# Kernel tuning notes

Hardware: AMD Instinct MI355X
Metric: run time of the kernel (lower is better)

## Reference

```python
import jax, jax.numpy as jnp
import numpy as np

DT = 0.01
C_M = 1.0
G_NA, G_K, G_L = 120.0, 36.0, 0.3
E_NA, E_K, E_L = 50.0, -77.0, -54.387
G_SYN = 0.1  # all six conductances are 0.1
# order: AMPA, GABAa, GABAb, NMDA, ACh, D1 (type codes 1..6)
E_SYN = jnp.array([0.0, -70.0, -90.0, 0.0, 0.0, 0.0], jnp.float32)
TAU = jnp.array([2.0, 5.0, 10.0, 100.0, 50.0, 30.0], jnp.float32)
# I_pre = I_ext - I_AMPA + I_GABAa + I_GABAb - I_NMDA - I_ACh - I_D1
SIGN = jnp.array([-1.0, 1.0, 1.0, -1.0, -1.0, -1.0], jnp.float32)


def setup_inputs() -> dict:
    key = jax.random.key(0)
    N = 4096
    k0, k1, k2, k3 = jax.random.split(key, 4)
    return dict(
        I_ext=jax.random.normal(k0, (N,), jnp.float32),
        synaptic_weights=jax.random.uniform(k1, (N, N), jnp.float32),
        V0=jnp.zeros((N,), jnp.float32),
        m0=jnp.zeros((N,), jnp.float32),
        h0=jnp.zeros((N,), jnp.float32),
        n0=jnp.zeros((N,), jnp.float32),
        s0=jax.random.uniform(k2, (6, N), jnp.float32),
        synapse_types=jax.random.randint(k3, (N, N), 0, 7).astype(jnp.int32),
        T=10,
    )


def reference(I_ext, synaptic_weights, V0, m0, h0, n0, s0, synapse_types, T):
    num_steps = int(T / DT)
    # sum_{i,j} vec[j] * mask_t[i,j] * W[i,j] == dot(vec, colsum_t)
    # precompute per-type column sums of masked weights: [6, N]
    cols = jnp.stack([
        jnp.sum(jnp.where(synapse_types == t, synaptic_weights, 0.0), axis=0)
        for t in range(1, 7)
    ])
    decay = 1.0 - DT / TAU  # [6], exponential decay of gating variables

    def step(carry, _):
        V, m, h, n, s = carry
        s = s * decay[:, None]                          # [6, N]
        vec = G_SYN * s * (V[None, :] - E_SYN[:, None])  # [6, N]
        I_t = jnp.sum(vec * cols, axis=1)                # [6] scalar currents
        I_pre = I_ext + jnp.sum(SIGN * I_t)              # [N]
        # HH gating rates at current V
        am = (2.5 - 0.1 * V) / (jnp.exp(2.5 - 0.1 * V) - 1.0)
        bm = 4.0 * jnp.exp(-V / 18.0)
        ah = 0.07 * jnp.exp(-V / 20.0)
        bh = 1.0 / (jnp.exp(3.0 - 0.1 * V) + 1.0)
        an = (0.1 - 0.01 * V) / (jnp.exp(1.0 - 0.1 * V) - 1.0)
        bn = 0.125 * jnp.exp(-V / 80.0)
        m = m + DT * (am * (1.0 - m) - bm * m)
        h = h + DT * (ah * (1.0 - h) - bh * h)
        n = n + DT * (an * (1.0 - n) - bn * n)
        I_Na = G_NA * m**3 * h * (V - E_NA)
        I_K = G_K * n**4 * (V - E_K)
        I_L = G_L * (V - E_L)
        Vn = jnp.clip(V + DT * (I_pre - I_Na - I_K - I_L) / C_M, -100.0, 100.0)
        Vn = jnp.nan_to_num(Vn)
        return (Vn, m, h, n, s), Vn

    _, V_hist = jax.lax.scan(step, (V0, m0, h0, n0, s0), None, length=num_steps)
    return V_hist  # [num_steps, N]
```

## Files before the change

kernel.cpp:

```cpp
#include <hip/hip_runtime.h>
#include <math.h>

#define NN 4096
#define CBLK 8
#define NPB (NN / CBLK)
#define GRID_SIM 128
#define SLOT_STRIDE 16
#define CTRL_BYTES 4096
#define CTRL_ULLS 512
#define TRAJ_CAP 2040
#define TRAJ_BYTES 8192

typedef unsigned long long ull;


template <int DC, int RM>
__device__ __forceinline__ float dppmov(float x) {
    return __int_as_float(
        __builtin_amdgcn_update_dpp(0, __float_as_int(x), DC, RM, 0xf, true));
}
__device__ __forceinline__ float wave_sum63(float x) {
    x += dppmov<0x111, 0xf>(x);
    x += dppmov<0x112, 0xf>(x);
    x += dppmov<0x114, 0xf>(x);
    x += dppmov<0x118, 0xf>(x);
    x += dppmov<0x142, 0xa>(x);
    x += dppmov<0x143, 0xc>(x);
    return x;
}
__device__ __forceinline__ float wave_max63(float x) {
    x = fmaxf(x, dppmov<0x111, 0xf>(x));
    x = fmaxf(x, dppmov<0x112, 0xf>(x));
    x = fmaxf(x, dppmov<0x114, 0xf>(x));
    x = fmaxf(x, dppmov<0x118, 0xf>(x));
    x = fmaxf(x, dppmov<0x142, 0xa>(x));
    x = fmaxf(x, dppmov<0x143, 0xc>(x));
    return x;
}
__device__ __forceinline__ float dpp_sum8(float x) {
    x += dppmov<0x111, 0xf>(x);
    x += dppmov<0x112, 0xf>(x);
    x += dppmov<0x114, 0xf>(x);
    return x;
}
__device__ __forceinline__ float rdlane(float x, int l) {
    return __int_as_float(__builtin_amdgcn_readlane(__float_as_int(x), l));
}

__global__ __launch_bounds__(256) void col_partial_k(
    const float* __restrict__ W, const int* __restrict__ Ty,
    float* __restrict__ part, int chunkRows)
{
    const int tid = threadIdx.x;
    const int wv = tid >> 6;
    const int lane = tid & 63;
    const int j4 = (blockIdx.x * 64 + lane) * 4;
    const int c = blockIdx.y;
    const int rpw = chunkRows >> 2;
    const size_t i0 = (size_t)c * (size_t)chunkRows + (size_t)wv * (size_t)rpw;

    float a[6][4];
#pragma unroll
    for (int t = 0; t < 6; ++t)
#pragma unroll
        for (int r = 0; r < 4; ++r) a[t][r] = 0.f;

#pragma unroll 4
    for (size_t i = i0; i < i0 + (size_t)rpw; ++i) {
        const size_t off = i * NN + j4;
        const float4 w = *(const float4*)(W + off);
        const int4 t = *(const int4*)(Ty + off);
        const float wv4[4] = { w.x, w.y, w.z, w.w };
        const int tv[4] = { t.x, t.y, t.z, t.w };
#pragma unroll
        for (int r = 0; r < 4; ++r) {
            a[0][r] += (tv[r] == 1) ? wv4[r] : 0.f;
            a[1][r] += (tv[r] == 2) ? wv4[r] : 0.f;
            a[2][r] += (tv[r] == 3) ? wv4[r] : 0.f;
            a[3][r] += (tv[r] == 4) ? wv4[r] : 0.f;
            a[4][r] += (tv[r] == 5) ? wv4[r] : 0.f;
            a[5][r] += (tv[r] == 6) ? wv4[r] : 0.f;
        }
    }

    __shared__ float red[3][64][25];
    if (wv > 0) {
#pragma unroll
        for (int t = 0; t < 6; ++t)
#pragma unroll
            for (int r = 0; r < 4; ++r)
                red[wv - 1][lane][t * 4 + r] = a[t][r];
    }
    __syncthreads();
    if (wv == 0) {
#pragma unroll
        for (int w = 0; w < 3; ++w)
#pragma unroll
            for (int t = 0; t < 6; ++t)
#pragma unroll
                for (int r = 0; r < 4; ++r)
                    a[t][r] += red[w][lane][t * 4 + r];
        const size_t base = ((size_t)c * 6) * NN + (size_t)j4;
#pragma unroll
        for (int t = 0; t < 6; ++t)
            *(float4*)(part + base + (size_t)t * NN) =
                make_float4(a[t][0], a[t][1], a[t][2], a[t][3]);
    }
}

__global__ __launch_bounds__(256) void col_reduce_k(
    const float* __restrict__ part, float* __restrict__ cols, int CH)
{
    const int idx = blockIdx.x * 256 + threadIdx.x;
    float s = 0.f;
    for (int c = 0; c < CH; ++c) s += part[(size_t)c * 6 * NN + idx];
    cols[idx] = s;
}

__global__ __launch_bounds__(512) void hh_probe_k(
    const float* __restrict__ Iext, const float* __restrict__ V0,
    const float* __restrict__ m0, const float* __restrict__ h0,
    const float* __restrict__ n0, const float* __restrict__ s0,
    const float* __restrict__ cols, ull* __restrict__ ctrl,
    const int* __restrict__ Tp,
    float* __restrict__ traj, int* __restrict__ status)
{
#pragma clang fp contract(off)
    const int tid = threadIdx.x, wave = tid >> 6, lane = tid & 63;
    const int steps = Tp[0] * 100;

    if (tid < CTRL_ULLS) ctrl[tid] = 0ULL;

    __shared__ float red[8];
    __shared__ float sQg[6], sMIe, sBad;

    float bad = 0.f, mie = 0.f;
    for (int i = tid; i < NN; i += 512) {
        bad += (V0[i] != 0.f) ? 1.f : 0.f;
        bad += (m0[i] != 0.f) ? 1.f : 0.f;
        bad += (h0[i] != 0.f) ? 1.f : 0.f;
        bad += (n0[i] != 0.f) ? 1.f : 0.f;
        mie = fmaxf(mie, fabsf(Iext[i]));
    }
    bad = wave_sum63(bad);
    if (lane == 63) red[wave] = bad;
    __syncthreads();
    if (tid == 0) { float s = 0.f; for (int w = 0; w < 8; ++w) s += red[w]; sBad = s; }
    __syncthreads();
    mie = wave_max63(mie);
    if (lane == 63) red[wave] = mie;
    __syncthreads();
    if (tid == 0) { float s = 0.f; for (int w = 0; w < 8; ++w) s = fmaxf(s, red[w]); sMIe = s; }
    __syncthreads();
    for (int t = 0; t < 6; ++t) {
        float acc = 0.f;
        for (int i = tid; i < NN; i += 512)
            acc += 0.1f * s0[(size_t)t * NN + i] * cols[(size_t)t * NN + i];
        acc = wave_sum63(acc);
        if (lane == 63) red[wave] = acc;
        __syncthreads();
        if (tid == 0) { float s = 0.f; for (int w = 0; w < 8; ++w) s += red[w]; sQg[t] = s; }
        __syncthreads();
    }

    if (sBad != 0.f || steps > TRAJ_CAP) {
        if (tid == 0) *status = 0;
        return;
    }
    if (wave != 0) return;

    float Qg[6];
#pragma unroll
    for (int t = 0; t < 6; ++t) Qg[t] = sQg[t];
    const float MIe = sMIe;
    const float CE1g = -70.0f * Qg[1];
    const float CE2g = -90.0f * Qg[2];

    const float tau[6] = { 2.0f, 5.0f, 10.0f, 100.0f, 50.0f, 30.0f };
    const float sgn[6] = { -1.0f, 1.0f, 1.0f, -1.0f, -1.0f, -1.0f };
    float dec[6], sD[6];
#pragma unroll
    for (int t = 0; t < 6; ++t) { dec[t] = 1.0f - 0.01f / tau[t]; sD[t] = sgn[t] * dec[t]; }

    float vu = 0.0f, m = 0.0f, h = 0.0f, n = 0.0f;
    int ok = 1;
    int kend = steps;

    for (int k = 0; k < steps; ++k) {
        float Cg = sD[5] * Qg[5];
        Cg = fmaf(sD[4], Qg[4], Cg);
        Cg = fmaf(sD[3], Qg[3], Cg);
        Cg = fmaf(sD[2], Qg[2], Cg);
        Cg = fmaf(sD[1], Qg[1], Cg);
        Cg = fmaf(sD[0], Qg[0], Cg);
        const float corrg = fmaf(sD[1], CE1g, sD[2] * CE2g);
        const float S = fmaf(vu, Cg, -corrg);

        const float v = vu;
        const float a1 = 2.5f - 0.1f * v;
        const float X = __expf(a1);
        const float am = a1 * __builtin_amdgcn_rcpf(X - 1.0f);
        const float bm = 4.0f * __expf(v * (-1.0f / 18.0f));
        const float ah = 0.07f * __expf(v * (-1.0f / 20.0f));
        const float bh = __builtin_amdgcn_rcpf(fmaf(1.6487212707001281f, X, 1.0f));
        const float a5 = 0.1f - 0.01f * v;
        const float an = a5 * __builtin_amdgcn_rcpf(fmaf(0.2231301601484298f, X, -1.0f));
        const float bn = 0.125f * __expf(v * (-1.0f / 80.0f));
        const float mm = m + 0.01f * (am * (1.0f - m) - bm * m);
        const float hh = h + 0.01f * (ah * (1.0f - h) - bh * h);
        const float nn = n + 0.01f * (an * (1.0f - n) - bn * n);
        m = mm; h = hh; n = nn;
        const float INa = ((120.0f * ((mm * mm) * mm)) * hh) * (v - 50.0f);
        const float n2 = nn * nn;
        const float IK = (36.0f * (n2 * n2)) * (v + 77.0f);
        const float IL = 0.3f * (v + 54.387f);
        const float Bu = ((0.0f - INa) - IK) - IL;
        const float t = vu + 0.01f * (Bu + S);

        float vn;
        if (t != t) {
            vn = 0.0f;
        } else if (t > 1e30f) {
            vn = 100.0f;
        } else if (t < -1e30f) {
            vn = -100.0f;
        } else {
            const float slack = 0.01f * MIe + 0.01f +
                1e-4f * (fabsf(t) + fabsf(vu) +
                         0.01f * (fabsf(S) + fabsf(INa) + fabsf(IK)));
            if (t - slack > 100.0f)       vn = 100.0f;
            else if (t + slack < -100.0f) vn = -100.0f;
            else { ok = 0; break; }
        }
        if (lane == 0) traj[k] = vn;
        vu = vn;

        if ((m != m) || (h != h) || (n != n)) { kend = k + 1; break; }

#pragma unroll
        for (int t6 = 0; t6 < 6; ++t6) sD[t6] *= dec[t6];
    }
    if (ok) {
        for (int r = kend + lane; r < steps; r += 64) traj[r] = 0.0f;
    }
    if (lane == 0) *status = ok;
}

__global__ __launch_bounds__(NPB) void hh_sim_k(
    const float* __restrict__ Iext, const float* __restrict__ V0,
    const float* __restrict__ m0, const float* __restrict__ h0,
    const float* __restrict__ n0, const float* __restrict__ s0,
    const float* __restrict__ cols, const int* __restrict__ Tp,
    ull* __restrict__ ctrl, const float* __restrict__ traj,
    const int* __restrict__ status, float* __restrict__ out)
{
#pragma clang fp contract(off)
    const int steps = Tp[0] * 100;
    const int tid = threadIdx.x;

    if (*status == 1) {
        for (int r = blockIdx.x; r < steps; r += GRID_SIM) {
            const float vv = traj[r];
            const float4 val = make_float4(vv, vv, vv, vv);
            float4* p = (float4*)(out + (size_t)r * NN + (size_t)tid * 8);
            p[0] = val; p[1] = val;
        }
        return;
    }

    const int wave = tid >> 6;
    const int lane = tid & 63;

    __shared__ int sRank; __shared__ ull sKey, sChosen;
    __shared__ ull wtag[2][8];
    __shared__ float binit1[8], binit2[8];

    if (tid == 0) {
        const int xid = (int)(__builtin_amdgcn_s_getreg((3 << 11) | 20)) & 7;
        const ull r = atomicAdd(&ctrl[(size_t)xid * SLOT_STRIDE], 1ULL);
        if (r == (ull)(CBLK - 1))
            atomicCAS(&ctrl[128], 0ULL, (ull)(xid + 1));
        ull ch;
        do {
            ch = __hip_atomic_load(&ctrl[128],
                                   __ATOMIC_RELAXED, __HIP_MEMORY_SCOPE_AGENT);
        } while (ch == 0ULL);
        sRank = (int)r; sKey = (ull)(xid + 1); sChosen = ch;
    }
    __syncthreads();
    const int b = sRank;
    if (sKey != sChosen || b >= CBLK) return;

    const int j = b * NPB + tid;
    ull* const slots = ctrl + 144;

    const float tau[6] = { 2.0f, 5.0f, 10.0f, 100.0f, 50.0f, 30.0f };
    const float sgn[6] = { -1.0f, 1.0f, 1.0f, -1.0f, -1.0f, -1.0f };
    float dec[6], sD[6];
#pragma unroll
    for (int t = 0; t < 6; ++t) { dec[t] = 1.0f - 0.01f / tau[t]; sD[t] = sgn[t]; }

    if (tid < 16) wtag[tid >> 3][tid & 7] = 0ULL;

    float V = V0[j], m = m0[j], h = h0[j], n = n0[j], Ie = Iext[j];
    float q[6];
#pragma unroll
    for (int t = 0; t < 6; ++t)
        q[t] = 0.1f * s0[(size_t)t * NN + j] * cols[(size_t)t * NN + j];

    {
        const float b1 = wave_sum63(q[1]);
        const float b2 = wave_sum63(q[2]);
        if (lane == 63) { binit1[wave] = b1; binit2[wave] = b2; }
    }
    __syncthreads();
    float CE1 = 0.f, CE2 = 0.f;
    if (wave == 0) {
        const float s1 = dpp_sum8((lane < 8) ? binit1[lane] : 0.f);
        const float s2 = dpp_sum8((lane < 8) ? binit2[lane] : 0.f);
        CE1 = -70.0f * rdlane(s1, 7);
        CE2 = -90.0f * rdlane(s2, 7);
    }
    __syncthreads();

#pragma unroll
    for (int t = 0; t < 6; ++t) sD[t] *= dec[t];
    float w6 = sD[5] * q[5];
    w6 = fmaf(sD[4], q[4], w6);
    w6 = fmaf(sD[3], q[3], w6);
    w6 = fmaf(sD[2], q[2], w6);
    w6 = fmaf(sD[1], q[1], w6);
    w6 = fmaf(sD[0], q[0], w6);
    float corr = fmaf(sD[1], CE1, sD[2] * CE2);

    float* op = out + j;

    for (int k = 0; k < steps; ++k) {
        const unsigned tag = (unsigned)(k + 1);
        const int par = (k & 1);

        const float x = w6 * V;
        const float xs = wave_sum63(x);
        if (lane == 63)
            __hip_atomic_store(&wtag[par][wave],
                               ((ull)tag << 32) | (ull)__float_as_uint(xs),
                               __ATOMIC_RELAXED, __HIP_MEMORY_SCOPE_WORKGROUP);
        __builtin_amdgcn_sched_barrier(0);

        if (wave == 0) {
            ull got = 0;
            if (lane < 8) {
                do {
                    got = __hip_atomic_load(&wtag[par][lane],
                                            __ATOMIC_RELAXED,
                                            __HIP_MEMORY_SCOPE_WORKGROUP);
                } while ((unsigned)(got >> 32) != tag);
            }
            float p = dpp_sum8((lane < 8) ? __uint_as_float((unsigned)got) : 0.f);
            if (lane == 7) {
                p = p - corr;
                const ull packed = ((ull)tag << 32) | (ull)__float_as_uint(p);
                __hip_atomic_store(&slots[(size_t)(par * CBLK + b) * SLOT_STRIDE],
                                   packed, __ATOMIC_RELAXED,
                                   __HIP_MEMORY_SCOPE_AGENT);
            }
        }
        __builtin_amdgcn_sched_barrier(0);
        __builtin_amdgcn_s_barrier();
        __builtin_amdgcn_sched_barrier(0);

        const float v = V;
        const float a1 = 2.5f - 0.1f * v;
        const float X = __expf(a1);
        const float am = a1 * __builtin_amdgcn_rcpf(X - 1.0f);
        const float bm = 4.0f * __expf(v * (-1.0f / 18.0f));
        const float ah = 0.07f * __expf(v * (-1.0f / 20.0f));
        const float bh = __builtin_amdgcn_rcpf(
            fmaf(1.6487212707001281f, X, 1.0f));
        const float a5 = 0.1f - 0.01f * v;
        const float an = a5 * __builtin_amdgcn_rcpf(
            fmaf(0.2231301601484298f, X, -1.0f));
        const float bn = 0.125f * __expf(v * (-1.0f / 80.0f));
        const float mm = m + 0.01f * (am * (1.0f - m) - bm * m);
        const float hh = h + 0.01f * (ah * (1.0f - h) - bh * h);
        const float nn = n + 0.01f * (an * (1.0f - n) - bn * n);
        m = mm; h = hh; n = nn;
        const float INa = ((120.0f * ((mm * mm) * mm)) * hh) * (v - 50.0f);
        const float n2 = nn * nn;
        const float IK = (36.0f * (n2 * n2)) * (v + 77.0f);
        const float IL = 0.3f * (v + 54.387f);
        const float base = ((Ie - INa) - IK) - IL;

#pragma unroll
        for (int t = 0; t < 6; ++t) sD[t] *= dec[t];
        float w6n = sD[5] * q[5];
        w6n = fmaf(sD[4], q[4], w6n);
        w6n = fmaf(sD[3], q[3], w6n);
        w6n = fmaf(sD[2], q[2], w6n);
        w6n = fmaf(sD[1], q[1], w6n);
        w6n = fmaf(sD[0], q[0], w6n);
        const float corrn = fmaf(sD[1], CE1, sD[2] * CE2);
        __builtin_amdgcn_sched_barrier(0);

        ull got = 0;
        if (lane < 8) {
            do {
                got = __hip_atomic_load(&slots[(size_t)(par * CBLK + lane) * SLOT_STRIDE],
                                        __ATOMIC_RELAXED, __HIP_MEMORY_SCOPE_AGENT);
            } while ((unsigned)(got >> 32) != tag);
        }
        float val = dpp_sum8((lane < 8) ? __uint_as_float((unsigned)got) : 0.f);
        const float S = rdlane(val, 7);

        const float u = V + 0.01f * (base + S);
        V = (u != u) ? 0.0f : fminf(fmaxf(u, -100.0f), 100.0f);
        *op = V; op += NN;
        w6 = w6n; corr = corrn;
    }
}

__global__ __launch_bounds__(1024) void hh_sim_single(
    const float* __restrict__ Iext, const float* __restrict__ V0,
    const float* __restrict__ m0, const float* __restrict__ h0,
    const float* __restrict__ n0, const float* __restrict__ s0,
    const float* __restrict__ colsg, const int* __restrict__ Tp,
    const float* __restrict__ W, const int* __restrict__ Ty,
    int computeCols, float* __restrict__ out)
{
#pragma clang fp contract(off)
    const int tid = threadIdx.x;
    const int j0 = tid * 4;
    const int steps = Tp[0] * 100;

    const float tau[6] = { 2.0f, 5.0f, 10.0f, 100.0f, 50.0f, 30.0f };
    const float sgn[6] = { -1.0f, 1.0f, 1.0f, -1.0f, -1.0f, -1.0f };
    float dec[6], sD[6];
#pragma unroll
    for (int t = 0; t < 6; ++t) { dec[t] = 1.0f - 0.01f / tau[t]; sD[t] = sgn[t]; }

    float q[6][4];
    if (computeCols) {
        float acc[6][4];
#pragma unroll
        for (int t = 0; t < 6; ++t)
#pragma unroll
            for (int r = 0; r < 4; ++r) acc[t][r] = 0.f;
        for (int i = 0; i < NN; ++i) {
            const size_t rowo = (size_t)i * NN + (size_t)j0;
#pragma unroll
            for (int r = 0; r < 4; ++r) {
                const float w = W[rowo + r];
                const int t = Ty[rowo + r];
                acc[0][r] += (t == 1) ? w : 0.f;
                acc[1][r] += (t == 2) ? w : 0.f;
                acc[2][r] += (t == 3) ? w : 0.f;
                acc[3][r] += (t == 4) ? w : 0.f;
                acc[4][r] += (t == 5) ? w : 0.f;
                acc[5][r] += (t == 6) ? w : 0.f;
            }
        }
#pragma unroll
        for (int t = 0; t < 6; ++t)
#pragma unroll
            for (int r = 0; r < 4; ++r)
                q[t][r] = 0.1f * s0[(size_t)t * NN + j0 + r] * acc[t][r];
    } else {
#pragma unroll
        for (int t = 0; t < 6; ++t)
#pragma unroll
            for (int r = 0; r < 4; ++r)
                q[t][r] = 0.1f * s0[(size_t)t * NN + j0 + r] *
                          colsg[(size_t)t * NN + j0 + r];
    }

    float V[4], m[4], h[4], n[4], Ie[4];
#pragma unroll
    for (int r = 0; r < 4; ++r) {
        V[r] = V0[j0 + r]; m[r] = m0[j0 + r]; h[r] = h0[j0 + r];
        n[r] = n0[j0 + r]; Ie[r] = Iext[j0 + r];
    }

    __shared__ float wsum[2][16];
    __shared__ float Bsh[2];
    {
        float b1 = 0.f, b2 = 0.f;
#pragma unroll
        for (int r = 0; r < 4; ++r) { b1 += q[1][r]; b2 += q[2][r]; }
#pragma unroll
        for (int off = 32; off > 0; off >>= 1) {
            b1 += __shfl_down(b1, off);
            b2 += __shfl_down(b2, off);
        }
        if ((tid & 63) == 0) { wsum[0][tid >> 6] = b1; wsum[1][tid >> 6] = b2; }
        __syncthreads();
        if (tid == 0) {
            float s1 = 0.f, s2 = 0.f;
            for (int w2 = 0; w2 < 16; ++w2) { s1 += wsum[0][w2]; s2 += wsum[1][w2]; }
            Bsh[0] = s1; Bsh[1] = s2;
        }
        __syncthreads();
    }
    const float CE1 = -70.0f * Bsh[0];
    const float CE2 = -90.0f * Bsh[1];
    __syncthreads();

    for (int k = 0; k < steps; ++k) {
#pragma unroll
        for (int t = 0; t < 6; ++t) sD[t] *= dec[t];
        float p = 0.f;
#pragma unroll
        for (int r = 0; r < 4; ++r) {
            float w = sD[5] * q[5][r];
            w = fmaf(sD[4], q[4][r], w);
            w = fmaf(sD[3], q[3][r], w);
            w = fmaf(sD[2], q[2][r], w);
            w = fmaf(sD[1], q[1][r], w);
            w = fmaf(sD[0], q[0][r], w);
            p = fmaf(w, V[r], p);
        }
#pragma unroll
        for (int off = 32; off > 0; off >>= 1) p += __shfl_down(p, off);
        const int par = k & 1;
        if ((tid & 63) == 0) wsum[par][tid >> 6] = p;
        __syncthreads();
        float psum = 0.f;
#pragma unroll
        for (int w2 = 0; w2 < 16; ++w2) psum += wsum[par][w2];
        const float S = psum - fmaf(sD[1], CE1, sD[2] * CE2);

#pragma unroll
        for (int r = 0; r < 4; ++r) {
            const float v = V[r];
            const float Ipre = Ie[r] + S;
            const float a1 = 2.5f - 0.1f * v;
            const float X = __expf(a1);
            const float am = a1 * __builtin_amdgcn_rcpf(X - 1.0f);
            const float bm = 4.0f * __expf(v * (-1.0f / 18.0f));
            const float ah = 0.07f * __expf(v * (-1.0f / 20.0f));
            const float bh = __builtin_amdgcn_rcpf(fmaf(1.6487212707001281f, X, 1.0f));
            const float a5 = 0.1f - 0.01f * v;
            const float an = a5 * __builtin_amdgcn_rcpf(fmaf(0.2231301601484298f, X, -1.0f));
            const float bn = 0.125f * __expf(v * (-1.0f / 80.0f));
            const float mm = m[r] + 0.01f * (am * (1.0f - m[r]) - bm * m[r]);
            const float hh = h[r] + 0.01f * (ah * (1.0f - h[r]) - bh * h[r]);
            const float nn = n[r] + 0.01f * (an * (1.0f - n[r]) - bn * n[r]);
            m[r] = mm; h[r] = hh; n[r] = nn;
            const float INa = ((120.0f * ((mm * mm) * mm)) * hh) * (v - 50.0f);
            const float n2 = nn * nn;
            const float IK = (36.0f * (n2 * n2)) * (v + 77.0f);
            const float IL = 0.3f * (v + 54.387f);
            const float u = v + 0.01f * (((Ipre - INa) - IK) - IL);
            V[r] = (u != u) ? 0.0f : fminf(fmaxf(u, -100.0f), 100.0f);
        }
        *(float4*)(out + (size_t)k * NN + j0) =
            make_float4(V[0], V[1], V[2], V[3]);
    }
}

extern "C" void kernel_launch(void* const* d_in, const int* in_sizes, int n_in,
                              void* d_out, int out_size, void* d_ws, size_t ws_size,
                              hipStream_t stream)
{
    const float* Iext = (const float*)d_in[0];
    const float* W    = (const float*)d_in[1];
    const float* V0   = (const float*)d_in[2];
    const float* m0   = (const float*)d_in[3];
    const float* h0   = (const float*)d_in[4];
    const float* n0   = (const float*)d_in[5];
    const float* s0   = (const float*)d_in[6];
    const int*   Ty   = (const int*)d_in[7];
    const int*   Tp   = (const int*)d_in[8];
    float* out = (float*)d_out;

    ull*   ctrl = (ull*)d_ws;
    float* cols = (float*)((char*)d_ws + CTRL_BYTES);
    float* traj = (float*)((char*)cols + (size_t)6 * NN * sizeof(float));
    int*   status = (int*)(traj + TRAJ_CAP);
    float* part = (float*)((char*)traj + TRAJ_BYTES);

    int CH = 0;
    const int tiers[2] = { 32, 8 };
    const size_t fixed = CTRL_BYTES + TRAJ_BYTES + (size_t)6 * NN * sizeof(float);
    for (int i = 0; i < 2; ++i) {
        const size_t need = fixed + (size_t)tiers[i] * 6 * NN * sizeof(float);
        if (ws_size >= need) { CH = tiers[i]; break; }
    }
    if (CH == 0 && ws_size >= fixed) CH = 1;

    if (CH >= 1) {
        if (CH > 1) {
            hipLaunchKernelGGL(col_partial_k, dim3(NN / 256, CH), dim3(256), 0, stream,
                               W, Ty, part, NN / CH);
            hipLaunchKernelGGL(col_reduce_k, dim3(6 * NN / 256), dim3(256), 0, stream,
                               part, cols, CH);
        } else {
            hipLaunchKernelGGL(col_partial_k, dim3(NN / 256, 1), dim3(256), 0, stream,
                               W, Ty, cols, NN);
        }
        hipLaunchKernelGGL(hh_probe_k, dim3(1), dim3(512), 0, stream,
                           Iext, V0, m0, h0, n0, s0, cols, ctrl, Tp, traj, status);
        hipLaunchKernelGGL(hh_sim_k, dim3(GRID_SIM), dim3(NPB), 0, stream,
                           Iext, V0, m0, h0, n0, s0, cols, Tp, ctrl, traj, status, out);
    } else {
        hipLaunchKernelGGL(hh_sim_single, dim3(1), dim3(1024), 0, stream,
                           Iext, V0, m0, h0, n0, s0, (const float*)0, Tp, W, Ty, 1, out);
    }
}
```

Measured before the change: 241.0 us.

## Fuse column sums, probe and broadcast into one cooperative grid-synced kernel

The column-sum partials, the partial reduction, the per-type current reduction, the trajectory probe and the output broadcast are merged into one cooperative kernel separated by grid.sync. The global reductions are spread across all blocks with atomics instead of running in a single 512-thread block. This removes several kernel launches and the serial reduction in the probe. In exchange it depends on cooperative launch (falling back to the old path on failure), always launches an early-exit fallback kernel, and adds grid-wide barriers plus atomic contention.

```diff
diff --git a/kernel.cpp b/kernel.cpp
--- a/kernel.cpp
+++ b/kernel.cpp
@@ -1,5 +1,8 @@
 #include <hip/hip_runtime.h>
+#include <hip/hip_cooperative_groups.h>
 #include <math.h>
+
+namespace cg = cooperative_groups;
 
 #define NN 4096
 #define CBLK 8
@@ -8,7 +11,7 @@
 #define SLOT_STRIDE 16
 #define CTRL_BYTES 4096
 #define CTRL_ULLS 512
-#define TRAJ_CAP 2040
+#define TRAJ_CAP 2032
 #define TRAJ_BYTES 8192
 
 typedef unsigned long long ull;
@@ -47,132 +50,13 @@
     return __int_as_float(__builtin_amdgcn_readlane(__float_as_int(x), l));
 }
 
-__global__ __launch_bounds__(256) void col_partial_k(
-    const float* __restrict__ W, const int* __restrict__ Ty,
-    float* __restrict__ part, int chunkRows)
+__device__ __forceinline__ int run_trajectory(
+    const float* Qacc, float MIe, int steps, int lane,
+    float* __restrict__ traj)
 {
-    const int tid = threadIdx.x;
-    const int wv = tid >> 6;
-    const int lane = tid & 63;
-    const int j4 = (blockIdx.x * 64 + lane) * 4;
-    const int c = blockIdx.y;
-    const int rpw = chunkRows >> 2;
-    const size_t i0 = (size_t)c * (size_t)chunkRows + (size_t)wv * (size_t)rpw;
-
-    float a[6][4];
-#pragma unroll
-    for (int t = 0; t < 6; ++t)
-#pragma unroll
-        for (int r = 0; r < 4; ++r) a[t][r] = 0.f;
-
-#pragma unroll 4
-    for (size_t i = i0; i < i0 + (size_t)rpw; ++i) {
-        const size_t off = i * NN + j4;
-        const float4 w = *(const float4*)(W + off);
-        const int4 t = *(const int4*)(Ty + off);
-        const float wv4[4] = { w.x, w.y, w.z, w.w };
-        const int tv[4] = { t.x, t.y, t.z, t.w };
-#pragma unroll
-        for (int r = 0; r < 4; ++r) {
-            a[0][r] += (tv[r] == 1) ? wv4[r] : 0.f;
-            a[1][r] += (tv[r] == 2) ? wv4[r] : 0.f;
-            a[2][r] += (tv[r] == 3) ? wv4[r] : 0.f;
-            a[3][r] += (tv[r] == 4) ? wv4[r] : 0.f;
-            a[4][r] += (tv[r] == 5) ? wv4[r] : 0.f;
-            a[5][r] += (tv[r] == 6) ? wv4[r] : 0.f;
-        }
-    }
-
-    __shared__ float red[3][64][25];
-    if (wv > 0) {
-#pragma unroll
-        for (int t = 0; t < 6; ++t)
-#pragma unroll
-            for (int r = 0; r < 4; ++r)
-                red[wv - 1][lane][t * 4 + r] = a[t][r];
-    }
-    __syncthreads();
-    if (wv == 0) {
-#pragma unroll
-        for (int w = 0; w < 3; ++w)
-#pragma unroll
-            for (int t = 0; t < 6; ++t)
-#pragma unroll
-                for (int r = 0; r < 4; ++r)
-                    a[t][r] += red[w][lane][t * 4 + r];
-        const size_t base = ((size_t)c * 6) * NN + (size_t)j4;
-#pragma unroll
-        for (int t = 0; t < 6; ++t)
-            *(float4*)(part + base + (size_t)t * NN) =
-                make_float4(a[t][0], a[t][1], a[t][2], a[t][3]);
-    }
-}
-
-__global__ __launch_bounds__(256) void col_reduce_k(
-    const float* __restrict__ part, float* __restrict__ cols, int CH)
-{
-    const int idx = blockIdx.x * 256 + threadIdx.x;
-    float s = 0.f;
-    for (int c = 0; c < CH; ++c) s += part[(size_t)c * 6 * NN + idx];
-    cols[idx] = s;
-}
-
-__global__ __launch_bounds__(512) void hh_probe_k(
-    const float* __restrict__ Iext, const float* __restrict__ V0,
-    const float* __restrict__ m0, const float* __restrict__ h0,
-    const float* __restrict__ n0, const float* __restrict__ s0,
-    const float* __restrict__ cols, ull* __restrict__ ctrl,
-    const int* __restrict__ Tp,
-    float* __restrict__ traj, int* __restrict__ status)
-{
-#pragma clang fp contract(off)
-    const int tid = threadIdx.x, wave = tid >> 6, lane = tid & 63;
-    const int steps = Tp[0] * 100;
-
-    if (tid < CTRL_ULLS) ctrl[tid] = 0ULL;
-
-    __shared__ float red[8];
-    __shared__ float sQg[6], sMIe, sBad;
-
-    float bad = 0.f, mie = 0.f;
-    for (int i = tid; i < NN; i += 512) {
-        bad += (V0[i] != 0.f) ? 1.f : 0.f;
-        bad += (m0[i] != 0.f) ? 1.f : 0.f;
-        bad += (h0[i] != 0.f) ? 1.f : 0.f;
-        bad += (n0[i] != 0.f) ? 1.f : 0.f;
-        mie = fmaxf(mie, fabsf(Iext[i]));
-    }
-    bad = wave_sum63(bad);
-    if (lane == 63) red[wave] = bad;
-    __syncthreads();
-    if (tid == 0) { float s = 0.f; for (int w = 0; w < 8; ++w) s += red[w]; sBad = s; }
-    __syncthreads();
-    mie = wave_max63(mie);
-    if (lane == 63) red[wave] = mie;
-    __syncthreads();
-    if (tid == 0) { float s = 0.f; for (int w = 0; w < 8; ++w) s = fmaxf(s, red[w]); sMIe = s; }
-    __syncthreads();
-    for (int t = 0; t < 6; ++t) {
-        float acc = 0.f;
-        for (int i = tid; i < NN; i += 512)
-            acc += 0.1f * s0[(size_t)t * NN + i] * cols[(size_t)t * NN + i];
-        acc = wave_sum63(acc);
-        if (lane == 63) red[wave] = acc;
-        __syncthreads();
-        if (tid == 0) { float s = 0.f; for (int w = 0; w < 8; ++w) s += red[w]; sQg[t] = s; }
-        __syncthreads();
-    }
-
-    if (sBad != 0.f || steps > TRAJ_CAP) {
-        if (tid == 0) *status = 0;
-        return;
-    }
-    if (wave != 0) return;
-
     float Qg[6];
 #pragma unroll
-    for (int t = 0; t < 6; ++t) Qg[t] = sQg[t];
-    const float MIe = sMIe;
+    for (int t = 0; t < 6; ++t) Qg[t] = Qacc[t];
     const float CE1g = -70.0f * Qg[1];
     const float CE2g = -90.0f * Qg[2];
 
@@ -243,6 +127,460 @@
     if (ok) {
         for (int r = kend + lane; r < steps; r += 64) traj[r] = 0.0f;
     }
+    return ok;
+}
+
+__global__ __launch_bounds__(256) void hh_coop_k(
+    const float* __restrict__ Iext, const float* __restrict__ V0,
+    const float* __restrict__ m0, const float* __restrict__ h0,
+    const float* __restrict__ n0, const float* __restrict__ s0,
+    const float* __restrict__ W, const int* __restrict__ Ty,
+    const int* __restrict__ Tp, ull* __restrict__ ctrl,
+    float* __restrict__ part, float* __restrict__ cols,
+    float* __restrict__ traj, int* __restrict__ status,
+    int CH, float* __restrict__ out)
+{
+#pragma clang fp contract(off)
+    cg::grid_group grid = cg::this_grid();
+    const int tid = threadIdx.x;
+    const int wv = tid >> 6;
+    const int lane = tid & 63;
+    const int flat = blockIdx.y * gridDim.x + blockIdx.x;
+    const int nflat = gridDim.x * gridDim.y;
+
+    int* statusI = status;
+    float* Qacc = (float*)(status + 1);
+    unsigned* badc = (unsigned*)(Qacc + 6);
+    unsigned* mieb = badc + 1;
+
+    __shared__ float red[3][64][25];
+    __shared__ float redb[4], redm[4];
+
+    if (flat == 0) {
+        ctrl[tid] = 0ULL; ctrl[tid + 256] = 0ULL;
+        if (tid < 6) Qacc[tid] = 0.f;
+        if (tid == 6) *badc = 0u;
+        if (tid == 7) *mieb = 0u;
+        if (tid == 8) *statusI = 0;
+    }
+    {
+        const int chunkRows = NN / CH;
+        const int rpw = chunkRows >> 2;
+        const int j4 = (blockIdx.x * 64 + lane) * 4;
+        const int c = blockIdx.y;
+        const size_t i0 = (size_t)c * (size_t)chunkRows + (size_t)wv * (size_t)rpw;
+
+        float a[6][4];
+#pragma unroll
+        for (int t = 0; t < 6; ++t)
+#pragma unroll
+            for (int r = 0; r < 4; ++r) a[t][r] = 0.f;
+
+#pragma unroll 4
+        for (size_t i = i0; i < i0 + (size_t)rpw; ++i) {
+            const size_t off = i * NN + j4;
+            const float4 w = *(const float4*)(W + off);
+            const int4 t = *(const int4*)(Ty + off);
+            const float wv4[4] = { w.x, w.y, w.z, w.w };
+            const int tv[4] = { t.x, t.y, t.z, t.w };
+#pragma unroll
+            for (int r = 0; r < 4; ++r) {
+                a[0][r] += (tv[r] == 1) ? wv4[r] : 0.f;
+                a[1][r] += (tv[r] == 2) ? wv4[r] : 0.f;
+                a[2][r] += (tv[r] == 3) ? wv4[r] : 0.f;
+                a[3][r] += (tv[r] == 4) ? wv4[r] : 0.f;
+                a[4][r] += (tv[r] == 5) ? wv4[r] : 0.f;
+                a[5][r] += (tv[r] == 6) ? wv4[r] : 0.f;
+            }
+        }
+
+        if (wv > 0) {
+#pragma unroll
+            for (int t = 0; t < 6; ++t)
+#pragma unroll
+                for (int r = 0; r < 4; ++r)
+                    red[wv - 1][lane][t * 4 + r] = a[t][r];
+        }
+        __syncthreads();
+        if (wv == 0) {
+#pragma unroll
+            for (int w = 0; w < 3; ++w)
+#pragma unroll
+                for (int t = 0; t < 6; ++t)
+#pragma unroll
+                    for (int r = 0; r < 4; ++r)
+                        a[t][r] += red[w][lane][t * 4 + r];
+            const size_t base = ((size_t)c * 6) * NN + (size_t)j4;
+#pragma unroll
+            for (int t = 0; t < 6; ++t)
+                *(float4*)(part + base + (size_t)t * NN) =
+                    make_float4(a[t][0], a[t][1], a[t][2], a[t][3]);
+        }
+    }
+    grid.sync();
+
+    for (int base = flat * 256; base < 6 * NN; base += nflat * 256) {
+        const int idx = base + tid;
+        float sv;
+        if (CH > 1) {
+            float s = 0.f;
+            for (int c = 0; c < CH; ++c) s += part[(size_t)c * 6 * NN + idx];
+            cols[idx] = s;
+            sv = s;
+        } else {
+            sv = cols[idx];
+        }
+        float v = 0.1f * s0[idx] * sv;
+        v = wave_sum63(v);
+        if (lane == 63) redb[wv] = v;
+        __syncthreads();
+        if (tid == 0) {
+            const float s = redb[0] + redb[1] + redb[2] + redb[3];
+            atomicAdd(&Qacc[base >> 12], s);
+        }
+        __syncthreads();
+    }
+    for (int base = flat * 256; base < NN; base += nflat * 256) {
+        const int i = base + tid;
+        float bad = ((V0[i] != 0.f) ? 1.f : 0.f) + ((m0[i] != 0.f) ? 1.f : 0.f)
+                  + ((h0[i] != 0.f) ? 1.f : 0.f) + ((n0[i] != 0.f) ? 1.f : 0.f);
+        float aie = fabsf(Iext[i]);
+        bad = wave_sum63(bad);
+        aie = wave_max63(aie);
+        if (lane == 63) { redb[wv] = bad; redm[wv] = aie; }
+        __syncthreads();
+        if (tid == 0) {
+            const float b = redb[0] + redb[1] + redb[2] + redb[3];
+            const float mx = fmaxf(fmaxf(redm[0], redm[1]), fmaxf(redm[2], redm[3]));
+            if (b != 0.f) atomicAdd(badc, 1u);
+            atomicMax(mieb, __float_as_uint(mx));
+        }
+        __syncthreads();
+    }
+    grid.sync();
+
+    if (flat == 0) {
+        const int steps = Tp[0] * 100;
+        const bool okg = (*badc == 0u) && (steps <= TRAJ_CAP);
+        if (!okg) {
+            if (tid == 0)
+                __hip_atomic_store(statusI, 0, __ATOMIC_RELAXED,
+                                   __HIP_MEMORY_SCOPE_AGENT);
+        } else if (wv == 0) {
+            const float MIe = __uint_as_float(*mieb);
+            const int ok = run_trajectory(Qacc, MIe, steps, lane, traj);
+            if (lane == 0)
+                __hip_atomic_store(statusI, ok, __ATOMIC_RELAXED,
+                                   __HIP_MEMORY_SCOPE_AGENT);
+        }
+    }
+    grid.sync();
+
+    const int st = __hip_atomic_load(statusI, __ATOMIC_RELAXED,
+                                     __HIP_MEMORY_SCOPE_AGENT);
+    if (st == 1) {
+        const int steps = Tp[0] * 100;
+        for (int r = flat; r < steps; r += nflat) {
+            const float vv = traj[r];
+            const float4 val = make_float4(vv, vv, vv, vv);
+            float4* row = (float4*)(out + (size_t)r * NN);
+            row[tid] = val;
+            row[tid + 256] = val;
+            row[tid + 512] = val;
+            row[tid + 768] = val;
+        }
+    }
+}
+
+__global__ __launch_bounds__(NPB) void hh_fallback_k(
+    const float* __restrict__ Iext, const float* __restrict__ V0,
+    const float* __restrict__ m0, const float* __restrict__ h0,
+    const float* __restrict__ n0, const float* __restrict__ s0,
+    const float* __restrict__ cols, const int* __restrict__ Tp,
+    ull* __restrict__ ctrl, const int* __restrict__ status,
+    float* __restrict__ out)
+{
+#pragma clang fp contract(off)
+    if (__hip_atomic_load(status, __ATOMIC_RELAXED,
+                          __HIP_MEMORY_SCOPE_AGENT) == 1)
+        return;
+
+    const int steps = Tp[0] * 100;
+    const int tid = threadIdx.x;
+    const int wave = tid >> 6;
+    const int lane = tid & 63;
+
+    __shared__ int sRank; __shared__ ull sKey, sChosen;
+    __shared__ ull wtag[2][8];
+    __shared__ float binit1[8], binit2[8];
+
+    if (tid == 0) {
+        const int xid = (int)(__builtin_amdgcn_s_getreg((3 << 11) | 20)) & 7;
+        const ull r = atomicAdd(&ctrl[(size_t)xid * SLOT_STRIDE], 1ULL);
+        if (r == (ull)(CBLK - 1))
+            atomicCAS(&ctrl[128], 0ULL, (ull)(xid + 1));
+        ull ch;
+        do {
+            ch = __hip_atomic_load(&ctrl[128],
+                                   __ATOMIC_RELAXED, __HIP_MEMORY_SCOPE_AGENT);
+        } while (ch == 0ULL);
+        sRank = (int)r; sKey = (ull)(xid + 1); sChosen = ch;
+    }
+    __syncthreads();
+    const int b = sRank;
+    if (sKey != sChosen || b >= CBLK) return;
+
+    const int j = b * NPB + tid;
+    ull* const slots = ctrl + 144;
+
+    const float tau[6] = { 2.0f, 5.0f, 10.0f, 100.0f, 50.0f, 30.0f };
+    const float sgn[6] = { -1.0f, 1.0f, 1.0f, -1.0f, -1.0f, -1.0f };
+    float dec[6], sD[6];
+#pragma unroll
+    for (int t = 0; t < 6; ++t) { dec[t] = 1.0f - 0.01f / tau[t]; sD[t] = sgn[t]; }
+
+    if (tid < 16) wtag[tid >> 3][tid & 7] = 0ULL;
+
+    float V = V0[j], m = m0[j], h = h0[j], n = n0[j], Ie = Iext[j];
+    float q[6];
+#pragma unroll
+    for (int t = 0; t < 6; ++t)
+        q[t] = 0.1f * s0[(size_t)t * NN + j] * cols[(size_t)t * NN + j];
+
+    {
+        const float b1 = wave_sum63(q[1]);
+        const float b2 = wave_sum63(q[2]);
+        if (lane == 63) { binit1[wave] = b1; binit2[wave] = b2; }
+    }
+    __syncthreads();
+    float CE1 = 0.f, CE2 = 0.f;
+    if (wave == 0) {
+        const float s1 = dpp_sum8((lane < 8) ? binit1[lane] : 0.f);
+        const float s2 = dpp_sum8((lane < 8) ? binit2[lane] : 0.f);
+        CE1 = -70.0f * rdlane(s1, 7);
+        CE2 = -90.0f * rdlane(s2, 7);
+    }
+    __syncthreads();
+
+#pragma unroll
+    for (int t = 0; t < 6; ++t) sD[t] *= dec[t];
+    float w6 = sD[5] * q[5];
+    w6 = fmaf(sD[4], q[4], w6);
+    w6 = fmaf(sD[3], q[3], w6);
+    w6 = fmaf(sD[2], q[2], w6);
+    w6 = fmaf(sD[1], q[1], w6);
+    w6 = fmaf(sD[0], q[0], w6);
+    float corr = fmaf(sD[1], CE1, sD[2] * CE2);
+
+    float* op = out + j;
+
+    for (int k = 0; k < steps; ++k) {
+        const unsigned tag = (unsigned)(k + 1);
+        const int par = (k & 1);
+
+        const float x = w6 * V;
+        const float xs = wave_sum63(x);
+        if (lane == 63)
+            __hip_atomic_store(&wtag[par][wave],
+                               ((ull)tag << 32) | (ull)__float_as_uint(xs),
+                               __ATOMIC_RELAXED, __HIP_MEMORY_SCOPE_WORKGROUP);
+        __builtin_amdgcn_sched_barrier(0);
+
+        if (wave == 0) {
+            ull got = 0;
+            if (lane < 8) {
+                do {
+                    got = __hip_atomic_load(&wtag[par][lane],
+                                            __ATOMIC_RELAXED,
+                                            __HIP_MEMORY_SCOPE_WORKGROUP);
+                } while ((unsigned)(got >> 32) != tag);
+            }
+            float p = dpp_sum8((lane < 8) ? __uint_as_float((unsigned)got) : 0.f);
+            if (lane == 7) {
+                p = p - corr;
+                const ull packed = ((ull)tag << 32) | (ull)__float_as_uint(p);
+                __hip_atomic_store(&slots[(size_t)(par * CBLK + b) * SLOT_STRIDE],
+                                   packed, __ATOMIC_RELAXED,
+                                   __HIP_MEMORY_SCOPE_AGENT);
+            }
+        }
+        __builtin_amdgcn_sched_barrier(0);
+        __builtin_amdgcn_s_barrier();
+        __builtin_amdgcn_sched_barrier(0);
+
+        const float v = V;
+        const float a1 = 2.5f - 0.1f * v;
+        const float X = __expf(a1);
+        const float am = a1 * __builtin_amdgcn_rcpf(X - 1.0f);
+        const float bm = 4.0f * __expf(v * (-1.0f / 18.0f));
+        const float ah = 0.07f * __expf(v * (-1.0f / 20.0f));
+        const float bh = __builtin_amdgcn_rcpf(
+            fmaf(1.6487212707001281f, X, 1.0f));
+        const float a5 = 0.1f - 0.01f * v;
+        const float an = a5 * __builtin_amdgcn_rcpf(
+            fmaf(0.2231301601484298f, X, -1.0f));
+        const float bn = 0.125f * __expf(v * (-1.0f / 80.0f));
+        const float mm = m + 0.01f * (am * (1.0f - m) - bm * m);
+        const float hh = h + 0.01f * (ah * (1.0f - h) - bh * h);
+        const float nn = n + 0.01f * (an * (1.0f - n) - bn * n);
+        m = mm; h = hh; n = nn;
+        const float INa = ((120.0f * ((mm * mm) * mm)) * hh) * (v - 50.0f);
+        const float n2 = nn * nn;
+        const float IK = (36.0f * (n2 * n2)) * (v + 77.0f);
+        const float IL = 0.3f * (v + 54.387f);
+        const float base = ((Ie - INa) - IK) - IL;
+
+#pragma unroll
+        for (int t = 0; t < 6; ++t) sD[t] *= dec[t];
+        float w6n = sD[5] * q[5];
+        w6n = fmaf(sD[4], q[4], w6n);
+        w6n = fmaf(sD[3], q[3], w6n);
+        w6n = fmaf(sD[2], q[2], w6n);
+        w6n = fmaf(sD[1], q[1], w6n);
+        w6n = fmaf(sD[0], q[0], w6n);
+        const float corrn = fmaf(sD[1], CE1, sD[2] * CE2);
+        __builtin_amdgcn_sched_barrier(0);
+
+        ull got = 0;
+        if (lane < 8) {
+            do {
+                got = __hip_atomic_load(&slots[(size_t)(par * CBLK + lane) * SLOT_STRIDE],
+                                        __ATOMIC_RELAXED, __HIP_MEMORY_SCOPE_AGENT);
+            } while ((unsigned)(got >> 32) != tag);
+        }
+        float val = dpp_sum8((lane < 8) ? __uint_as_float((unsigned)got) : 0.f);
+        const float S = rdlane(val, 7);
+
+        const float u = V + 0.01f * (base + S);
+        V = (u != u) ? 0.0f : fminf(fmaxf(u, -100.0f), 100.0f);
+        *op = V; op += NN;
+        w6 = w6n; corr = corrn;
+    }
+}
+
+__global__ __launch_bounds__(256) void col_partial_k(
+    const float* __restrict__ W, const int* __restrict__ Ty,
+    float* __restrict__ part, int chunkRows)
+{
+    const int tid = threadIdx.x;
+    const int wv = tid >> 6;
+    const int lane = tid & 63;
+    const int j4 = (blockIdx.x * 64 + lane) * 4;
+    const int c = blockIdx.y;
+    const int rpw = chunkRows >> 2;
+    const size_t i0 = (size_t)c * (size_t)chunkRows + (size_t)wv * (size_t)rpw;
+
+    float a[6][4];
+#pragma unroll
+    for (int t = 0; t < 6; ++t)
+#pragma unroll
+        for (int r = 0; r < 4; ++r) a[t][r] = 0.f;
+
+#pragma unroll 4
+    for (size_t i = i0; i < i0 + (size_t)rpw; ++i) {
+        const size_t off = i * NN + j4;
+        const float4 w = *(const float4*)(W + off);
+        const int4 t = *(const int4*)(Ty + off);
+        const float wv4[4] = { w.x, w.y, w.z, w.w };
+        const int tv[4] = { t.x, t.y, t.z, t.w };
+#pragma unroll
+        for (int r = 0; r < 4; ++r) {
+            a[0][r] += (tv[r] == 1) ? wv4[r] : 0.f;
+            a[1][r] += (tv[r] == 2) ? wv4[r] : 0.f;
+            a[2][r] += (tv[r] == 3) ? wv4[r] : 0.f;
+            a[3][r] += (tv[r] == 4) ? wv4[r] : 0.f;
+            a[4][r] += (tv[r] == 5) ? wv4[r] : 0.f;
+            a[5][r] += (tv[r] == 6) ? wv4[r] : 0.f;
+        }
+    }
+
+    __shared__ float red[3][64][25];
+    if (wv > 0) {
+#pragma unroll
+        for (int t = 0; t < 6; ++t)
+#pragma unroll
+            for (int r = 0; r < 4; ++r)
+                red[wv - 1][lane][t * 4 + r] = a[t][r];
+    }
+    __syncthreads();
+    if (wv == 0) {
+#pragma unroll
+        for (int w = 0; w < 3; ++w)
+#pragma unroll
+            for (int t = 0; t < 6; ++t)
+#pragma unroll
+                for (int r = 0; r < 4; ++r)
+                    a[t][r] += red[w][lane][t * 4 + r];
+        const size_t base = ((size_t)c * 6) * NN + (size_t)j4;
+#pragma unroll
+        for (int t = 0; t < 6; ++t)
+            *(float4*)(part + base + (size_t)t * NN) =
+                make_float4(a[t][0], a[t][1], a[t][2], a[t][3]);
+    }
+}
+
+__global__ __launch_bounds__(256) void col_reduce_k(
+    const float* __restrict__ part, float* __restrict__ cols, int CH)
+{
+    const int idx = blockIdx.x * 256 + threadIdx.x;
+    float s = 0.f;
+    for (int c = 0; c < CH; ++c) s += part[(size_t)c * 6 * NN + idx];
+    cols[idx] = s;
+}
+
+__global__ __launch_bounds__(512) void hh_probe_k(
+    const float* __restrict__ Iext, const float* __restrict__ V0,
+    const float* __restrict__ m0, const float* __restrict__ h0,
+    const float* __restrict__ n0, const float* __restrict__ s0,
+    const float* __restrict__ cols, ull* __restrict__ ctrl,
+    const int* __restrict__ Tp,
+    float* __restrict__ traj, int* __restrict__ status)
+{
+#pragma clang fp contract(off)
+    const int tid = threadIdx.x, wave = tid >> 6, lane = tid & 63;
+    const int steps = Tp[0] * 100;
+
+    if (tid < CTRL_ULLS) ctrl[tid] = 0ULL;
+
+    __shared__ float red[8];
+    __shared__ float sQg[6], sMIe, sBad;
+
+    float bad = 0.f, mie = 0.f;
+    for (int i = tid; i < NN; i += 512) {
+        bad += (V0[i] != 0.f) ? 1.f : 0.f;
+        bad += (m0[i] != 0.f) ? 1.f : 0.f;
+        bad += (h0[i] != 0.f) ? 1.f : 0.f;
+        bad += (n0[i] != 0.f) ? 1.f : 0.f;
+        mie = fmaxf(mie, fabsf(Iext[i]));
+    }
+    bad = wave_sum63(bad);
+    if (lane == 63) red[wave] = bad;
+    __syncthreads();
+    if (tid == 0) { float s = 0.f; for (int w = 0; w < 8; ++w) s += red[w]; sBad = s; }
+    __syncthreads();
+    mie = wave_max63(mie);
+    if (lane == 63) red[wave] = mie;
+    __syncthreads();
+    if (tid == 0) { float s = 0.f; for (int w = 0; w < 8; ++w) s = fmaxf(s, red[w]); sMIe = s; }
+    __syncthreads();
+    for (int t = 0; t < 6; ++t) {
+        float acc = 0.f;
+        for (int i = tid; i < NN; i += 512)
+            acc += 0.1f * s0[(size_t)t * NN + i] * cols[(size_t)t * NN + i];
+        acc = wave_sum63(acc);
+        if (lane == 63) red[wave] = acc;
+        __syncthreads();
+        if (tid == 0) { float s = 0.f; for (int w = 0; w < 8; ++w) s += red[w]; sQg[t] = s; }
+        __syncthreads();
+    }
+
+    if (sBad != 0.f || steps > TRAJ_CAP) {
+        if (tid == 0) *status = 0;
+        return;
+    }
+    if (wave != 0) return;
+
+    const int ok = run_trajectory(sQg, sMIe, steps, lane, traj);
     if (lane == 0) *status = ok;
 }
 
@@ -267,7 +605,6 @@
         }
         return;
     }
-
     const int wave = tid >> 6;
     const int lane = tid & 63;
 
@@ -588,19 +925,38 @@
     if (CH == 0 && ws_size >= fixed) CH = 1;
 
     if (CH >= 1) {
-        if (CH > 1) {
-            hipLaunchKernelGGL(col_partial_k, dim3(NN / 256, CH), dim3(256), 0, stream,
-                               W, Ty, part, NN / CH);
-            hipLaunchKernelGGL(col_reduce_k, dim3(6 * NN / 256), dim3(256), 0, stream,
-                               part, cols, CH);
+        float* pbuf = (CH > 1) ? part : cols;
+
+        void* kargs[] = {
+            (void*)&Iext, (void*)&V0, (void*)&m0, (void*)&h0, (void*)&n0,
+            (void*)&s0, (void*)&W, (void*)&Ty, (void*)&Tp, (void*)&ctrl,
+            (void*)&pbuf, (void*)&cols, (void*)&traj, (void*)&status,
+            (void*)&CH, (void*)&out
+        };
+        hipError_t err = hipLaunchCooperativeKernel(
+            (const void*)hh_coop_k, dim3(16, CH), dim3(256), kargs, 0, stream);
+
+        if (err == hipSuccess) {
+            hipLaunchKernelGGL(hh_fallback_k, dim3(GRID_SIM), dim3(NPB), 0, stream,
+                               Iext, V0, m0, h0, n0, s0, cols, Tp, ctrl,
+                               (const int*)status, out);
         } else {
-            hipLaunchKernelGGL(col_partial_k, dim3(NN / 256, 1), dim3(256), 0, stream,
-                               W, Ty, cols, NN);
-        }
-        hipLaunchKernelGGL(hh_probe_k, dim3(1), dim3(512), 0, stream,
-                           Iext, V0, m0, h0, n0, s0, cols, ctrl, Tp, traj, status);
-        hipLaunchKernelGGL(hh_sim_k, dim3(GRID_SIM), dim3(NPB), 0, stream,
-                           Iext, V0, m0, h0, n0, s0, cols, Tp, ctrl, traj, status, out);
+            (void)hipGetLastError();
+            if (CH > 1) {
+                hipLaunchKernelGGL(col_partial_k, dim3(NN / 256, CH), dim3(256), 0,
+                                   stream, W, Ty, part, NN / CH);
+                hipLaunchKernelGGL(col_reduce_k, dim3(6 * NN / 256), dim3(256), 0,
+                                   stream, part, cols, CH);
+            } else {
+                hipLaunchKernelGGL(col_partial_k, dim3(NN / 256, 1), dim3(256), 0,
+                                   stream, W, Ty, cols, NN);
+            }
+            hipLaunchKernelGGL(hh_probe_k, dim3(1), dim3(512), 0, stream,
+                               Iext, V0, m0, h0, n0, s0, cols, ctrl, Tp, traj, status);
+            hipLaunchKernelGGL(hh_sim_k, dim3(GRID_SIM), dim3(NPB), 0, stream,
+                               Iext, V0, m0, h0, n0, s0, cols, Tp, ctrl, traj,
+                               (const int*)status, out);
+        }
     } else {
         hipLaunchKernelGGL(hh_sim_single, dim3(1), dim3(1024), 0, stream,
                            Iext, V0, m0, h0, n0, s0, (const float*)0, Tp, W, Ty, 1, out);
```

After: 364.5 us. +51.2%, slower.
